# Kernel optimization log

Measured on AMD Instinct MI355X. Metric: run time of the kernel, lower is better.

The kernel has to match this reference:

```python
import jax, jax.numpy as jnp
import numpy as np

N, F, H, C, E = 100000, 128, 64, 16, 1000000


def _prop(x, src, dst, w):
    # gather source features, scale by edge weight, scatter-add to destinations
    msgs = x[src] * w[:, None]  # [E, H]
    return jax.ops.segment_sum(msgs, dst, num_segments=N)


def _gru(x, h, W_ih, W_hh, b_ih, b_hh):
    gi = x @ W_ih.T + b_ih  # [N, 3H]
    gh = h @ W_hh.T + b_hh
    i_r, i_z, i_n = jnp.split(gi, 3, axis=1)
    h_r, h_z, h_n = jnp.split(gh, 3, axis=1)
    r = jax.nn.sigmoid(i_r + h_r)
    z = jax.nn.sigmoid(i_z + h_z)
    n = jnp.tanh(i_n + r * h_n)
    return (1.0 - z) * n + z * h


def setup_inputs() -> dict:
    key = jax.random.key(0)
    ks = jax.random.split(key, 20)
    s = 0.05
    inp = {
        'x': jax.random.normal(ks[0], (N, F), jnp.float32),
        'edge_index': jax.random.randint(ks[1], (2, E), 0, N),
        'edge_weight': jax.random.uniform(ks[2], (E,), jnp.float32),
        'edge_index_re': jax.random.randint(ks[3], (2, E), 0, N),
        'edge_weight_re': jax.random.uniform(ks[4], (E,), jnp.float32),
        'W_first': jax.random.normal(ks[5], (H, F), jnp.float32) * s,
        'b_first': jnp.zeros((H,), jnp.float32),
        'W_con1': jax.random.normal(ks[6], (H, 2 * H), jnp.float32) * s,
        'b_con1': jnp.zeros((H,), jnp.float32),
        'W_con2': jax.random.normal(ks[7], (H, 2 * H), jnp.float32) * s,
        'b_con2': jnp.zeros((H,), jnp.float32),
        'W_lin1': jax.random.normal(ks[8], (H, H), jnp.float32) * s,
        'b_lin1': jnp.zeros((H,), jnp.float32),
        'W_out': jax.random.normal(ks[9], (C, H), jnp.float32) * s,
        'b_out': jnp.zeros((C,), jnp.float32),
        'W_ih': jax.random.normal(ks[10], (3 * H, H), jnp.float32) * s,
        'W_hh': jax.random.normal(ks[11], (3 * H, H), jnp.float32) * s,
        'b_ih': jnp.zeros((3 * H,), jnp.float32),
        'b_hh': jnp.zeros((3 * H,), jnp.float32),
    }
    return inp


def reference(x, edge_index, edge_weight, edge_index_re, edge_weight_re,
              W_first, b_first, W_con1, b_con1, W_con2, b_con2,
              W_lin1, b_lin1, W_out, b_out, W_ih, W_hh, b_ih, b_hh):
    src, dst = edge_index[0], edge_index[1]
    src_r, dst_r = edge_index_re[0], edge_index_re[1]

    x = x @ W_first.T + b_first  # [N, H]; dropout is identity at inference
    h = x

    x1 = _prop(x, src, dst, edge_weight)
    x2 = _prop(x, src_r, dst_r, edge_weight_re)
    x = jnp.concatenate([x1, x2], axis=1) @ W_con1.T + b_con1
    x = _gru(x, h, W_ih, W_hh, b_ih, b_hh)
    x = x @ W_lin1.T + b_lin1

    x1 = _prop(x, src, dst, edge_weight)
    x2 = _prop(x, src_r, dst_r, edge_weight_re)
    x = jnp.concatenate([x1, x2], axis=1) @ W_con2.T + b_con2
    x = _gru(x, h, W_ih, W_hh, b_ih, b_hh)
    x = x @ W_out.T + b_out
    return jax.nn.log_softmax(x, axis=-1)
```

## Files before the change

kernel.cpp:

```cpp
#include <hip/hip_runtime.h>

#define NN 100000
#define FF 128
#define HH 64
#define CC 16
#define EE 1000000
#define NSEG (2*NN)
#define BSH 11
#define BKD  (1 << BSH)
#define NBUK ((NSEG + BKD - 1) / BKD)
#define EPB 4096
#define P1BLK ((2*EE + EPB - 1) / EPB)
#define PRE_TOT (192*128 + 192 + 192*64 + 64*128 + 64*64 + 16*64)
#define PRE_BLK ((PRE_TOT + 255)/256)
#define LIN_TILES ((NN + 31)/32)
#define LINB ((LIN_TILES + 3)/4)

typedef __bf16 bf16;
typedef __attribute__((ext_vector_type(8))) __bf16 bf16x8;
typedef __attribute__((ext_vector_type(4))) __bf16 bf16x4;
typedef __attribute__((ext_vector_type(4))) float f32x4;
typedef __attribute__((ext_vector_type(2))) float f32x2;

__device__ __forceinline__ float fsig(float t)  { return 1.0f/(1.0f+__expf(-t)); }
__device__ __forceinline__ float ftanh(float t) { return 1.0f - 2.0f/(__expf(2.0f*t)+1.0f); }

__device__ __forceinline__ unsigned pack_sw(int s, float w) {
    unsigned short u = __builtin_bit_cast(unsigned short, (bf16)w);
    return ((unsigned)s << 15) | (u & 0x7FFFu);
}

__device__ __forceinline__ void precomp_body(int idx,
                               const float* __restrict__ W_ih, const float* __restrict__ b_ih,
                               const float* __restrict__ Wc1,  const float* __restrict__ bc1,
                               const float* __restrict__ Wc2,  const float* __restrict__ bc2,
                               const float* __restrict__ W_hh, const float* __restrict__ W_first,
                               const float* __restrict__ W_lin1, const float* __restrict__ W_out,
                               bf16* __restrict__ W1bf, float* __restrict__ b1,
                               bf16* __restrict__ W2bf, float* __restrict__ b2,
                               bf16* __restrict__ Whbf, bf16* __restrict__ Wfbf,
                               bf16* __restrict__ Wlbf, bf16* __restrict__ Wobf)
{
    const int t0 = 192*128;
    const int t1 = t0 + 192;
    const int t2 = t1 + 192*64;
    const int t3 = t2 + 64*128;
    const int t4 = t3 + 64*64;
    const int t5 = t4 + 16*64;
    if (idx < t0) {
        int j = idx >> 7, k = idx & 127;
        float s1 = 0.f, s2 = 0.f;
        for (int m=0; m<64; ++m) {
            float wih = W_ih[j*64+m];
            s1 += wih * Wc1[m*128+k];
            s2 += wih * Wc2[m*128+k];
        }
        W1bf[idx] = (bf16)s1; W2bf[idx] = (bf16)s2;
    } else if (idx < t1) {
        int j = idx - t0;
        float s1 = b_ih[j], s2 = b_ih[j];
        for (int m=0; m<64; ++m) {
            float wih = W_ih[j*64+m];
            s1 += wih * bc1[m];
            s2 += wih * bc2[m];
        }
        b1[j] = s1; b2[j] = s2;
    } else if (idx < t2) {
        int i = idx - t1;  Whbf[i] = (bf16)W_hh[i];
    } else if (idx < t3) {
        int i = idx - t2;  Wfbf[i] = (bf16)W_first[i];
    } else if (idx < t4) {
        int i = idx - t3;  Wlbf[i] = (bf16)W_lin1[i];
    } else if (idx < t5) {
        int i = idx - t4;  Wobf[i] = (bf16)W_out[i];
    }
}

__global__ __launch_bounds__(256) void count_precomp_kernel(
    const int* __restrict__ ei, const int* __restrict__ ei_re, int* __restrict__ bkcnt,
    const float* __restrict__ W_ih, const float* __restrict__ b_ih,
    const float* __restrict__ Wc1,  const float* __restrict__ bc1,
    const float* __restrict__ Wc2,  const float* __restrict__ bc2,
    const float* __restrict__ W_hh, const float* __restrict__ W_first,
    const float* __restrict__ W_lin1, const float* __restrict__ W_out,
    bf16* __restrict__ W1bf, float* __restrict__ b1,
    bf16* __restrict__ W2bf, float* __restrict__ b2,
    bf16* __restrict__ Whbf, bf16* __restrict__ Wfbf,
    bf16* __restrict__ Wlbf, bf16* __restrict__ Wobf)
{
    __shared__ int hist[NBUK];
    const int t = threadIdx.x;
    if (blockIdx.x < P1BLK) {
        for (int i=t; i<NBUK; i+=256) hist[i] = 0;
        __syncthreads();
        const long e0 = (long)blockIdx.x * EPB;
        #pragma unroll
        for (int it=0; it<16; ++it) {
            long e = e0 + it*256 + t;
            int d = -1;
            if (e < EE)        d = ei[EE + e];
            else if (e < 2*EE) d = NN + ei_re[EE + (e - EE)];
            if (d >= 0) atomicAdd(&hist[d >> BSH], 1);
        }
        __syncthreads();
        for (int i=t; i<NBUK; i+=256) if (hist[i]) atomicAdd(&bkcnt[i], hist[i]);
    } else {
        int idx = (blockIdx.x - P1BLK)*256 + t;
        precomp_body(idx, W_ih, b_ih, Wc1, bc1, Wc2, bc2, W_hh, W_first, W_lin1, W_out,
                     W1bf, b1, W2bf, b2, Whbf, Wfbf, Wlbf, Wobf);
    }
}

__global__ void bucket_scan_kernel(const int* __restrict__ bkcnt,
                                   int* __restrict__ bkbase, int* __restrict__ bkcur,
                                   int* __restrict__ rp)
{
    __shared__ int sc[128];
    const int t = threadIdx.x;
    int v = (t < NBUK) ? bkcnt[t] : 0;
    sc[t] = v;
    __syncthreads();
    #pragma unroll
    for (int off=1; off<128; off<<=1) {
        int x = (t>=off) ? sc[t-off] : 0;
        __syncthreads();
        sc[t] += x;
        __syncthreads();
    }
    int excl = sc[t] - v;
    if (t < NBUK) { bkbase[t] = excl; bkcur[t] = excl; }
    if (t == NBUK-1) bkbase[NBUK] = sc[t];
    if (t == 0) rp[NSEG] = 2*EE;
}

__global__ __launch_bounds__(256) void fillA_kernel(const int* __restrict__ ei,
                                                    const float* __restrict__ ew,
                                                    const int* __restrict__ ei_re,
                                                    const float* __restrict__ ew_re,
                                                    int* __restrict__ bkcur,
                                                    int* __restrict__ tmp_d,
                                                    unsigned* __restrict__ tmp_p)
{
    __shared__ int hist[NBUK];
    __shared__ int base[NBUK];
    const int t = threadIdx.x;
    for (int i=t; i<NBUK; i+=256) hist[i] = 0;
    __syncthreads();
    const long e0 = (long)blockIdx.x * EPB;
    int pr[16];
    #pragma unroll
    for (int it=0; it<16; ++it) {
        long e = e0 + it*256 + t;
        int d = -1;
        if (e < EE)        d = ei[EE + e];
        else if (e < 2*EE) d = NN + ei_re[EE + (e - EE)];
        if (d >= 0) {
            int b = d >> BSH;
            int r = atomicAdd(&hist[b], 1);
            pr[it] = (b << 16) | r;
        } else pr[it] = -1;
    }
    __syncthreads();
    for (int i=t; i<NBUK; i+=256) base[i] = atomicAdd(&bkcur[i], hist[i]);
    __syncthreads();
    #pragma unroll
    for (int it=0; it<16; ++it) {
        if (pr[it] < 0) continue;
        long e = e0 + it*256 + t;
        int d, s; float w;
        if (e < EE) { d = ei[EE+e]; s = ei[e]; w = ew[e]; }
        else { long j = e - EE; d = NN + ei_re[EE+j]; s = ei_re[j]; w = ew_re[j]; }
        int pos = base[pr[it] >> 16] + (pr[it] & 0xFFFF);
        tmp_d[pos] = d;
        tmp_p[pos] = pack_sw(s, w);
    }
}

__global__ __launch_bounds__(1024) void fillB_lin_kernel(
    const int* __restrict__ bkbase,
    const int* __restrict__ tmp_d, const unsigned* __restrict__ tmp_p,
    unsigned* __restrict__ edata, int* __restrict__ rp,
    const float* __restrict__ X, const bf16* __restrict__ Wf,
    const float* __restrict__ bfirst, float* __restrict__ Y, bf16* __restrict__ Ybf)
{
    __shared__ __align__(16) char smem[4*32*136*2];
    const int t = threadIdx.x;
    if (blockIdx.x < NBUK) {
        int* cntL  = (int*)smem;
        int* scanL = (int*)(smem + BKD*4);
        const int b  = blockIdx.x;
        const int d0 = b << BSH;
        const int dn = min(BKD, NSEG - d0);
        const int p0 = bkbase[b];
        const int p1 = bkbase[b+1];
        for (int i=t; i<BKD; i+=1024) cntL[i] = 0;
        __syncthreads();
        for (int pos = p0 + t; pos < p1; pos += 1024)
            atomicAdd(&cntL[tmp_d[pos] - d0], 1);
        __syncthreads();
        int a0 = cntL[2*t], a1 = cntL[2*t+1];
        int ps = a0 + a1;
        scanL[t] = ps;
        __syncthreads();
        #pragma unroll
        for (int off=1; off<1024; off<<=1) {
            int x = (t>=off) ? scanL[t-off] : 0;
            __syncthreads();
            scanL[t] += x;
            __syncthreads();
        }
        int g0 = p0 + scanL[t] - ps;
        int g1 = g0 + a0;
        if (2*t   < dn) rp[d0 + 2*t]   = g0;
        if (2*t+1 < dn) rp[d0 + 2*t+1] = g1;
        cntL[2*t]   = g0;
        cntL[2*t+1] = g1;
        __syncthreads();
        for (int pos = p0 + t; pos < p1; pos += 1024) {
            int d = tmp_d[pos];
            int p = atomicAdd(&cntL[d - d0], 1);
            edata[p] = tmp_p[pos];
        }
    } else {
        const int lb   = blockIdx.x - NBUK;
        const int sub  = t >> 8;
        const int tt   = t & 255;
        const int tile = lb*4 + sub;
        const bool valid = tile < LIN_TILES;
        const int tb = tile * 32;
        const int w = tt >> 6, lane = tt & 63, col = lane & 15, quad = lane >> 4;
        bf16* Alds = (bf16*)smem + sub*(32*136);
        bf16x8 B[4];
        #pragma unroll
        for (int ks=0; ks<4; ++ks)
            B[ks] = *(const bf16x8*)&Wf[(16*w+col)*128 + ks*32 + quad*8];
        const float bv = bfirst[16*w + col];
        const int m_st = tt >> 3, c_in = tt & 7;
        if (valid) {
            const float4* rx = (const float4*)&X[(long)(tb+m_st)*FF];
            #pragma unroll
            for (int it=0; it<4; ++it) {
                int cc = c_in + it*8;
                float4 v = rx[cc];
                bf16x4 bvv = {(bf16)v.x,(bf16)v.y,(bf16)v.z,(bf16)v.w};
                *(bf16x4*)&Alds[m_st*136 + cc*4] = bvv;
            }
        }
        __syncthreads();
        f32x4 acc[2] = {{0.f,0.f,0.f,0.f},{0.f,0.f,0.f,0.f}};
        #pragma unroll
        for (int ks=0; ks<4; ++ks)
            #pragma unroll
            for (int mt=0; mt<2; ++mt) {
                bf16x8 a = *(const bf16x8*)&Alds[(mt*16+col)*136 + ks*32+quad*8];
                acc[mt] = __builtin_amdgcn_mfma_f32_16x16x32_bf16(a, B[ks], acc[mt], 0,0,0);
            }
        if (valid) {
            #pragma unroll
            for (int mt=0; mt<2; ++mt)
                #pragma unroll
                for (int r=0; r<4; ++r) {
                    long n = tb + mt*16 + quad*4 + r;
                    float val = acc[mt][r] + bv;
                    Y  [n*HH + 16*w+col] = val;
                    Ybf[n*HH + 16*w+col] = (bf16)val;
                }
        }
    }
}

__global__ __launch_bounds__(256) void csr_prop_kernel(const bf16* __restrict__ X,
    const int* __restrict__ rp, const unsigned* __restrict__ edata,
    bf16* __restrict__ x1, bf16* __restrict__ x2)
{
    int s = blockIdx.x*4 + (threadIdx.x>>6);
    if (s >= NSEG) return;
    const int lane = threadIdx.x & 63;
    const int q  = lane >> 4;
    const int fl = lane & 15;
    const unsigned foff = 8u*(unsigned)fl;
    const int e0 = rp[s], e1 = rp[s+1];
    const char* Xb = (const char*)X;
    const char* Eb = (const char*)edata;

    f32x2 acc01 = {0.f, 0.f}, acc23 = {0.f, 0.f};
    int eq = e0 + q;
    unsigned eqb = 4u*(unsigned)eq;
    for (int base = e0; base < e1; base += 16, eq += 16, eqb += 64u) {
        const int rem = e1 - eq;
        #pragma unroll
        for (int j=0; j<4; ++j) {
            unsigned p = *(const unsigned*)(Eb + (eqb + 16u*(unsigned)j));
            const bool v = (4*j < rem);
            float w = v ? __uint_as_float((p & 0x7FFFu) << 16) : 0.f;
            unsigned voff = v ? (((p >> 8) & 0xFFFFFF80u) | foff) : foff;
            uint2 d = *(const uint2*)(Xb + voff);
            f32x2 lo = { __uint_as_float(d.x << 16), __uint_as_float(d.x & 0xFFFF0000u) };
            f32x2 hi = { __uint_as_float(d.y << 16), __uint_as_float(d.y & 0xFFFF0000u) };
            f32x2 w2 = { w, w };
            acc01 += w2 * lo;
            acc23 += w2 * hi;
        }
    }
    float a0 = acc01.x, a1 = acc01.y, a2 = acc23.x, a3 = acc23.y;
    a0 += __shfl_xor(a0, 32); a0 += __shfl_xor(a0, 16);
    a1 += __shfl_xor(a1, 32); a1 += __shfl_xor(a1, 16);
    a2 += __shfl_xor(a2, 32); a2 += __shfl_xor(a2, 16);
    a3 += __shfl_xor(a3, 32); a3 += __shfl_xor(a3, 16);
    if (q == 0) {
        bf16* o = (s < NN) ? &x1[(long)s*HH] : &x2[(long)(s-NN)*HH];
        bf16x4 ov = {(bf16)a0, (bf16)a1, (bf16)a2, (bf16)a3};
        *(bf16x4*)&o[4*fl] = ov;
    }
}

template<int MODE>
__global__ __launch_bounds__(256, 2) void layer_fused_kernel(
    const bf16* __restrict__ X1, const bf16* __restrict__ X2,
    const float* __restrict__ H, const bf16* __restrict__ Hbf,
    const bf16* __restrict__ Wg, const float* __restrict__ bg,
    const bf16* __restrict__ Wh, const float* __restrict__ bh,
    const bf16* __restrict__ Ws, const float* __restrict__ bs,
    bf16* __restrict__ Obf, float* __restrict__ Of)
{
    const int t    = threadIdx.x;
    const int w    = t >> 6;
    const int lane = t & 63;
    const int col  = lane & 15;
    const int quad = lane >> 4;

    bf16x8 Bg[3][4];
    bf16x8 Bh[3][2];
    float bgv[3], bhv[3];
    #pragma unroll
    for (int jt=0; jt<3; ++jt) {
        int J = jt*64 + 16*w + col;
        #pragma unroll
        for (int ks=0; ks<4; ++ks)
            Bg[jt][ks] = *(const bf16x8*)&Wg[J*128 + ks*32 + quad*8];
        #pragma unroll
        for (int ks=0; ks<2; ++ks)
            Bh[jt][ks] = *(const bf16x8*)&Wh[J*64 + ks*32 + quad*8];
        bgv[jt] = bg[J];
        bhv[jt] = bh[J];
    }

    bf16x8 B2[2];
    float b2s;
    if constexpr (MODE == 0) {
        #pragma unroll
        for (int ks=0; ks<2; ++ks)
            B2[ks] = *(const bf16x8*)&Ws[(16*w+col)*64 + ks*32 + quad*8];
        b2s = bs[16*w + col];
    } else {
        #pragma unroll
        for (int ks=0; ks<2; ++ks)
            B2[ks] = *(const bf16x8*)&Ws[col*64 + ks*32 + quad*8];
        b2s = bs[col];
    }

    __shared__ bf16 Alds[32][200];
    __shared__ bf16 Glds[32][72];

    const int m_st = t >> 3;
    const int c_in = t & 7;

    for (int tb = blockIdx.x*32; tb < NN; tb += gridDim.x*32) {
        {
            long n = tb + m_st;
            *(bf16x8*)&Alds[m_st][c_in*8]       = *(const bf16x8*)&X1[n*HH + c_in*8];
            *(bf16x8*)&Alds[m_st][64 + c_in*8]  = *(const bf16x8*)&X2[n*HH + c_in*8];
            *(bf16x8*)&Alds[m_st][128 + c_in*8] = *(const bf16x8*)&Hbf[n*HH + c_in*8];
        }
        __syncthreads();

        f32x4 accg[2][3];
        f32x4 acch[2][3];
        #pragma unroll
        for (int mt=0; mt<2; ++mt)
            #pragma unroll
            for (int jt=0; jt<3; ++jt) {
                accg[mt][jt] = (f32x4){0.f,0.f,0.f,0.f};
                acch[mt][jt] = (f32x4){0.f,0.f,0.f,0.f};
            }

        #pragma unroll
        for (int ks=0; ks<4; ++ks) {
            #pragma unroll
            for (int mt=0; mt<2; ++mt) {
                bf16x8 a = *(const bf16x8*)&Alds[mt*16 + col][ks*32 + quad*8];
                #pragma unroll
                for (int jt=0; jt<3; ++jt)
                    accg[mt][jt] = __builtin_amdgcn_mfma_f32_16x16x32_bf16(
                        a, Bg[jt][ks], accg[mt][jt], 0, 0, 0);
            }
        }
        #pragma unroll
        for (int ks=0; ks<2; ++ks) {
            #pragma unroll
            for (int mt=0; mt<2; ++mt) {
                bf16x8 a = *(const bf16x8*)&Alds[mt*16 + col][128 + ks*32 + quad*8];
                #pragma unroll
                for (int jt=0; jt<3; ++jt)
                    acch[mt][jt] = __builtin_amdgcn_mfma_f32_16x16x32_bf16(
                        a, Bh[jt][ks], acch[mt][jt], 0, 0, 0);
            }
        }

        const int c = 16*w + col;
        #pragma unroll
        for (int mt=0; mt<2; ++mt) {
            #pragma unroll
            for (int r=0; r<4; ++r) {
                long n = tb + mt*16 + quad*4 + r;
                float gr = accg[mt][0][r] + bgv[0];
                float gz = accg[mt][1][r] + bgv[1];
                float gn = accg[mt][2][r] + bgv[2];
                float hr = acch[mt][0][r] + bhv[0];
                float hz = acch[mt][1][r] + bhv[1];
                float hn = acch[mt][2][r] + bhv[2];
                float rr = fsig(gr + hr);
                float zz = fsig(gz + hz);
                float nv = ftanh(gn + rr*hn);
                float hv = H[n*HH + c];
                Glds[mt*16 + quad*4 + r][c] = (bf16)((1.0f - zz)*nv + zz*hv);
            }
        }
        __syncthreads();

        if constexpr (MODE == 0) {
            f32x4 acc2[2] = {{0.f,0.f,0.f,0.f},{0.f,0.f,0.f,0.f}};
            #pragma unroll
            for (int ks=0; ks<2; ++ks)
                #pragma unroll
                for (int mt=0; mt<2; ++mt) {
                    bf16x8 a = *(const bf16x8*)&Glds[mt*16+col][ks*32+quad*8];
                    acc2[mt] = __builtin_amdgcn_mfma_f32_16x16x32_bf16(a, B2[ks], acc2[mt], 0,0,0);
                }
            #pragma unroll
            for (int mt=0; mt<2; ++mt)
                #pragma unroll
                for (int r=0; r<4; ++r)
                    Obf[(long)(tb+mt*16+quad*4+r)*HH + 16*w+col] = (bf16)(acc2[mt][r] + b2s);
        } else {
            if (w < 2) {
                f32x4 acc2 = {0.f,0.f,0.f,0.f};
                #pragma unroll
                for (int ks=0; ks<2; ++ks) {
                    bf16x8 a = *(const bf16x8*)&Glds[w*16+col][ks*32+quad*8];
                    acc2 = __builtin_amdgcn_mfma_f32_16x16x32_bf16(a, B2[ks], acc2, 0,0,0);
                }
                #pragma unroll
                for (int r=0; r<4; ++r) {
                    long n = tb + w*16 + quad*4 + r;
                    float val = acc2[r] + b2s;
                    float m = val;
                    #pragma unroll
                    for (int off=8; off>0; off>>=1) m = fmaxf(m, __shfl_xor(m, off, 16));
                    float ex = __expf(val - m);
                    float ssum = ex;
                    #pragma unroll
                    for (int off=8; off>0; off>>=1) ssum += __shfl_xor(ssum, off, 16);
                    Of[n*CC + col] = val - m - __logf(ssum);
                }
            }
        }
    }
}

extern "C" void kernel_launch(void* const* d_in, const int* in_sizes, int n_in,
                              void* d_out, int out_size, void* d_ws, size_t ws_size,
                              hipStream_t stream)
{
    const float* x       = (const float*)d_in[0];
    const int*   ei      = (const int*)  d_in[1];
    const float* ew      = (const float*)d_in[2];
    const int*   ei_re   = (const int*)  d_in[3];
    const float* ew_re   = (const float*)d_in[4];
    const float* W_first = (const float*)d_in[5];
    const float* b_first = (const float*)d_in[6];
    const float* W_con1  = (const float*)d_in[7];
    const float* b_con1  = (const float*)d_in[8];
    const float* W_con2  = (const float*)d_in[9];
    const float* b_con2  = (const float*)d_in[10];
    const float* W_lin1  = (const float*)d_in[11];
    const float* b_lin1  = (const float*)d_in[12];
    const float* W_out   = (const float*)d_in[13];
    const float* b_out   = (const float*)d_in[14];
    const float* W_ih    = (const float*)d_in[15];
    const float* W_hh    = (const float*)d_in[16];
    const float* b_ih    = (const float*)d_in[17];
    const float* b_hh    = (const float*)d_in[18];
    float* out = (float*)d_out;

    float* h    = (float*)d_ws;
    bf16*  x1b  = (bf16*)(h + (long)NN*HH);
    bf16*  x2b  = x1b + (long)NN*HH;
    bf16*  hbf  = x2b + (long)NN*HH;
    bf16*  hAbf = hbf + (long)NN*HH;
    float* b1 = (float*)(hAbf + (long)NN*HH);
    float* b2 = b1 + 192;
    bf16*  W1bf = (bf16*)(b2 + 192);
    bf16*  W2bf = W1bf + 192*128;
    bf16*  Whbf = W2bf + 192*128;
    bf16*  Wfbf = Whbf + 192*64;
    bf16*  Wlbf = Wfbf + 64*128;
    bf16*  Wobf = Wlbf + 64*64;
    unsigned* edata = (unsigned*)(Wobf + 16*64);
    int*   rp     = (int*)(edata + 2*EE);
    int*   bkcnt  = rp + NSEG + 1;
    int*   bkbase = bkcnt + NBUK;
    int*   bkcur  = bkbase + NBUK + 1;
    int*      tmp_d = (int*)x1b;
    unsigned* tmp_p = (unsigned*)x2b;

    hipMemsetAsync(bkcnt, 0, (size_t)NBUK*sizeof(int), stream);
    count_precomp_kernel<<<P1BLK + PRE_BLK, 256, 0, stream>>>(
        ei, ei_re, bkcnt,
        W_ih, b_ih, W_con1, b_con1, W_con2, b_con2, W_hh, W_first, W_lin1, W_out,
        W1bf, b1, W2bf, b2, Whbf, Wfbf, Wlbf, Wobf);

    bucket_scan_kernel<<<1, 128, 0, stream>>>(bkcnt, bkbase, bkcur, rp);

    fillA_kernel<<<P1BLK, 256, 0, stream>>>(ei, ew, ei_re, ew_re, bkcur, tmp_d, tmp_p);

    fillB_lin_kernel<<<NBUK + LINB, 1024, 0, stream>>>(
        bkbase, tmp_d, tmp_p, edata, rp, x, Wfbf, b_first, h, hbf);

    csr_prop_kernel<<<(NSEG + 3)/4, 256, 0, stream>>>(hbf, rp, edata, x1b, x2b);

    layer_fused_kernel<0><<<1024, 256, 0, stream>>>(x1b, x2b, h, hbf, W1bf, b1, Whbf, b_hh,
                                                    Wlbf, b_lin1, hAbf, nullptr);

    csr_prop_kernel<<<(NSEG + 3)/4, 256, 0, stream>>>(hAbf, rp, edata, x1b, x2b);

    layer_fused_kernel<1><<<1024, 256, 0, stream>>>(x1b, x2b, h, hbf, W2bf, b2, Whbf, b_hh,
                                                    Wobf, b_out, nullptr, out);
}
```

Baseline: 380.5 us.

## Fold bucket scan into fill kernels, grid-stride CSR prop, stage H in LDS

Removes the single-block bucket_scan launch by having each fillA and fillB block redo the 98-entry prefix scan over bucket counts locally. This saves a kernel launch and a serial dependency at the cost of redundant per-block scans and extra barriers. The CSR propagation kernel becomes a grid-stride loop with a fixed 2048-block grid instead of one wave per segment row. The GRU layer now loads fp32 H once into LDS and converts it to bf16 there, replacing separate reads of the bf16 and fp32 copies of h.

```diff
diff --git a/kernel.cpp b/kernel.cpp
--- a/kernel.cpp
+++ b/kernel.cpp
@@ -15,6 +15,7 @@
 #define PRE_BLK ((PRE_TOT + 255)/256)
 #define LIN_TILES ((NN + 31)/32)
 #define LINB ((LIN_TILES + 3)/4)
+#define CSRB 2048
 
 typedef __bf16 bf16;
 typedef __attribute__((ext_vector_type(8))) __bf16 bf16x8;
@@ -111,40 +112,22 @@
     }
 }
 
-__global__ void bucket_scan_kernel(const int* __restrict__ bkcnt,
-                                   int* __restrict__ bkbase, int* __restrict__ bkcur,
-                                   int* __restrict__ rp)
-{
-    __shared__ int sc[128];
-    const int t = threadIdx.x;
-    int v = (t < NBUK) ? bkcnt[t] : 0;
-    sc[t] = v;
-    __syncthreads();
-    #pragma unroll
-    for (int off=1; off<128; off<<=1) {
-        int x = (t>=off) ? sc[t-off] : 0;
-        __syncthreads();
-        sc[t] += x;
-        __syncthreads();
-    }
-    int excl = sc[t] - v;
-    if (t < NBUK) { bkbase[t] = excl; bkcur[t] = excl; }
-    if (t == NBUK-1) bkbase[NBUK] = sc[t];
-    if (t == 0) rp[NSEG] = 2*EE;
-}
-
 __global__ __launch_bounds__(256) void fillA_kernel(const int* __restrict__ ei,
                                                     const float* __restrict__ ew,
                                                     const int* __restrict__ ei_re,
                                                     const float* __restrict__ ew_re,
+                                                    const int* __restrict__ bkcnt,
                                                     int* __restrict__ bkcur,
                                                     int* __restrict__ tmp_d,
                                                     unsigned* __restrict__ tmp_p)
 {
     __shared__ int hist[NBUK];
     __shared__ int base[NBUK];
+    __shared__ int sc[128];
     const int t = threadIdx.x;
     for (int i=t; i<NBUK; i+=256) hist[i] = 0;
+    int v = 0;
+    if (t < 128) { v = (t < NBUK) ? bkcnt[t] : 0; sc[t] = v; }
     __syncthreads();
     const long e0 = (long)blockIdx.x * EPB;
     int pr[16];
@@ -161,7 +144,17 @@
         } else pr[it] = -1;
     }
     __syncthreads();
-    for (int i=t; i<NBUK; i+=256) base[i] = atomicAdd(&bkcur[i], hist[i]);
+    #pragma unroll
+    for (int off=1; off<128; off<<=1) {
+        int x = 0;
+        if (t >= off && t < 128) x = sc[t-off];
+        __syncthreads();
+        if (t < 128) sc[t] += x;
+        __syncthreads();
+    }
+    if (t < 128 && t < NBUK) base[t] = sc[t] - v;
+    __syncthreads();
+    for (int i=t; i<NBUK; i+=256) base[i] += atomicAdd(&bkcur[i], hist[i]);
     __syncthreads();
     #pragma unroll
     for (int it=0; it<16; ++it) {
@@ -177,7 +170,7 @@
 }
 
 __global__ __launch_bounds__(1024) void fillB_lin_kernel(
-    const int* __restrict__ bkbase,
+    const int* __restrict__ bkcnt,
     const int* __restrict__ tmp_d, const unsigned* __restrict__ tmp_p,
     unsigned* __restrict__ edata, int* __restrict__ rp,
     const float* __restrict__ X, const bf16* __restrict__ Wf,
@@ -188,13 +181,24 @@
     if (blockIdx.x < NBUK) {
         int* cntL  = (int*)smem;
         int* scanL = (int*)(smem + BKD*4);
+        int* sc98  = (int*)(smem + BKD*4 + 4096);
         const int b  = blockIdx.x;
         const int d0 = b << BSH;
         const int dn = min(BKD, NSEG - d0);
-        const int p0 = bkbase[b];
-        const int p1 = bkbase[b+1];
+        if (b == 0 && t == 0) rp[NSEG] = 2*EE;
+        if (t < 128) sc98[t] = (t < NBUK) ? bkcnt[t] : 0;
         for (int i=t; i<BKD; i+=1024) cntL[i] = 0;
         __syncthreads();
+        #pragma unroll
+        for (int off=1; off<128; off<<=1) {
+            int x = 0;
+            if (t >= off && t < 128) x = sc98[t-off];
+            __syncthreads();
+            if (t < 128) sc98[t] += x;
+            __syncthreads();
+        }
+        const int p0 = (b == 0) ? 0 : sc98[b-1];
+        const int p1 = sc98[b];
         for (int pos = p0 + t; pos < p1; pos += 1024)
             atomicAdd(&cntL[tmp_d[pos] - d0], 1);
         __syncthreads();
@@ -273,51 +277,51 @@
     const int* __restrict__ rp, const unsigned* __restrict__ edata,
     bf16* __restrict__ x1, bf16* __restrict__ x2)
 {
-    int s = blockIdx.x*4 + (threadIdx.x>>6);
-    if (s >= NSEG) return;
     const int lane = threadIdx.x & 63;
     const int q  = lane >> 4;
     const int fl = lane & 15;
     const unsigned foff = 8u*(unsigned)fl;
-    const int e0 = rp[s], e1 = rp[s+1];
     const char* Xb = (const char*)X;
     const char* Eb = (const char*)edata;
 
-    f32x2 acc01 = {0.f, 0.f}, acc23 = {0.f, 0.f};
-    int eq = e0 + q;
-    unsigned eqb = 4u*(unsigned)eq;
-    for (int base = e0; base < e1; base += 16, eq += 16, eqb += 64u) {
-        const int rem = e1 - eq;
-        #pragma unroll
-        for (int j=0; j<4; ++j) {
-            unsigned p = *(const unsigned*)(Eb + (eqb + 16u*(unsigned)j));
-            const bool v = (4*j < rem);
-            float w = v ? __uint_as_float((p & 0x7FFFu) << 16) : 0.f;
-            unsigned voff = v ? (((p >> 8) & 0xFFFFFF80u) | foff) : foff;
-            uint2 d = *(const uint2*)(Xb + voff);
-            f32x2 lo = { __uint_as_float(d.x << 16), __uint_as_float(d.x & 0xFFFF0000u) };
-            f32x2 hi = { __uint_as_float(d.y << 16), __uint_as_float(d.y & 0xFFFF0000u) };
-            f32x2 w2 = { w, w };
-            acc01 += w2 * lo;
-            acc23 += w2 * hi;
-        }
-    }
-    float a0 = acc01.x, a1 = acc01.y, a2 = acc23.x, a3 = acc23.y;
-    a0 += __shfl_xor(a0, 32); a0 += __shfl_xor(a0, 16);
-    a1 += __shfl_xor(a1, 32); a1 += __shfl_xor(a1, 16);
-    a2 += __shfl_xor(a2, 32); a2 += __shfl_xor(a2, 16);
-    a3 += __shfl_xor(a3, 32); a3 += __shfl_xor(a3, 16);
-    if (q == 0) {
-        bf16* o = (s < NN) ? &x1[(long)s*HH] : &x2[(long)(s-NN)*HH];
-        bf16x4 ov = {(bf16)a0, (bf16)a1, (bf16)a2, (bf16)a3};
-        *(bf16x4*)&o[4*fl] = ov;
+    for (int s = blockIdx.x*4 + (threadIdx.x>>6); s < NSEG; s += gridDim.x*4) {
+        const int e0 = rp[s], e1 = rp[s+1];
+        f32x2 acc01 = {0.f, 0.f}, acc23 = {0.f, 0.f};
+        int eq = e0 + q;
+        unsigned eqb = 4u*(unsigned)eq;
+        for (int base = e0; base < e1; base += 16, eq += 16, eqb += 64u) {
+            const int rem = e1 - eq;
+            #pragma unroll
+            for (int j=0; j<4; ++j) {
+                unsigned p = *(const unsigned*)(Eb + (eqb + 16u*(unsigned)j));
+                const bool v = (4*j < rem);
+                float w = v ? __uint_as_float((p & 0x7FFFu) << 16) : 0.f;
+                unsigned voff = v ? (((p >> 8) & 0xFFFFFF80u) | foff) : foff;
+                uint2 d = *(const uint2*)(Xb + voff);
+                f32x2 lo = { __uint_as_float(d.x << 16), __uint_as_float(d.x & 0xFFFF0000u) };
+                f32x2 hi = { __uint_as_float(d.y << 16), __uint_as_float(d.y & 0xFFFF0000u) };
+                f32x2 w2 = { w, w };
+                acc01 += w2 * lo;
+                acc23 += w2 * hi;
+            }
+        }
+        float a0 = acc01.x, a1 = acc01.y, a2 = acc23.x, a3 = acc23.y;
+        a0 += __shfl_xor(a0, 32); a0 += __shfl_xor(a0, 16);
+        a1 += __shfl_xor(a1, 32); a1 += __shfl_xor(a1, 16);
+        a2 += __shfl_xor(a2, 32); a2 += __shfl_xor(a2, 16);
+        a3 += __shfl_xor(a3, 32); a3 += __shfl_xor(a3, 16);
+        if (q == 0) {
+            bf16* o = (s < NN) ? &x1[(long)s*HH] : &x2[(long)(s-NN)*HH];
+            bf16x4 ov = {(bf16)a0, (bf16)a1, (bf16)a2, (bf16)a3};
+            *(bf16x4*)&o[4*fl] = ov;
+        }
     }
 }
 
 template<int MODE>
 __global__ __launch_bounds__(256, 2) void layer_fused_kernel(
     const bf16* __restrict__ X1, const bf16* __restrict__ X2,
-    const float* __restrict__ H, const bf16* __restrict__ Hbf,
+    const float* __restrict__ H,
     const bf16* __restrict__ Wg, const float* __restrict__ bg,
     const bf16* __restrict__ Wh, const float* __restrict__ bh,
     const bf16* __restrict__ Ws, const float* __restrict__ bs,
@@ -359,8 +363,9 @@
         b2s = bs[col];
     }
 
-    __shared__ bf16 Alds[32][200];
-    __shared__ bf16 Glds[32][72];
+    __shared__ bf16  Alds[32][200];
+    __shared__ bf16  Glds[32][72];
+    __shared__ float Hlds[32][66];
 
     const int m_st = t >> 3;
     const int c_in = t & 7;
@@ -368,9 +373,15 @@
     for (int tb = blockIdx.x*32; tb < NN; tb += gridDim.x*32) {
         {
             long n = tb + m_st;
-            *(bf16x8*)&Alds[m_st][c_in*8]       = *(const bf16x8*)&X1[n*HH + c_in*8];
-            *(bf16x8*)&Alds[m_st][64 + c_in*8]  = *(const bf16x8*)&X2[n*HH + c_in*8];
-            *(bf16x8*)&Alds[m_st][128 + c_in*8] = *(const bf16x8*)&Hbf[n*HH + c_in*8];
+            *(bf16x8*)&Alds[m_st][c_in*8]      = *(const bf16x8*)&X1[n*HH + c_in*8];
+            *(bf16x8*)&Alds[m_st][64 + c_in*8] = *(const bf16x8*)&X2[n*HH + c_in*8];
+            const float4* rh = (const float4*)&H[n*HH];
+            float4 a = rh[c_in*2], b4 = rh[c_in*2+1];
+            bf16x8 hb = {(bf16)a.x,(bf16)a.y,(bf16)a.z,(bf16)a.w,
+                         (bf16)b4.x,(bf16)b4.y,(bf16)b4.z,(bf16)b4.w};
+            *(bf16x8*)&Alds[m_st][128 + c_in*8] = hb;
+            *(float4*)&Hlds[m_st][c_in*8]     = a;
+            *(float4*)&Hlds[m_st][c_in*8 + 4] = b4;
         }
         __syncthreads();
 
@@ -412,7 +423,6 @@
         for (int mt=0; mt<2; ++mt) {
             #pragma unroll
             for (int r=0; r<4; ++r) {
-                long n = tb + mt*16 + quad*4 + r;
                 float gr = accg[mt][0][r] + bgv[0];
                 float gz = accg[mt][1][r] + bgv[1];
                 float gn = accg[mt][2][r] + bgv[2];
@@ -422,7 +432,7 @@
                 float rr = fsig(gr + hr);
                 float zz = fsig(gz + hz);
                 float nv = ftanh(gn + rr*hn);
-                float hv = H[n*HH + c];
+                float hv = Hlds[mt*16 + quad*4 + r][c];
                 Glds[mt*16 + quad*4 + r][c] = (bf16)((1.0f - zz)*nv + zz*hv);
             }
         }
@@ -509,31 +519,28 @@
     unsigned* edata = (unsigned*)(Wobf + 16*64);
     int*   rp     = (int*)(edata + 2*EE);
     int*   bkcnt  = rp + NSEG + 1;
-    int*   bkbase = bkcnt + NBUK;
-    int*   bkcur  = bkbase + NBUK + 1;
+    int*   bkcur  = bkcnt + NBUK;
     int*      tmp_d = (int*)x1b;
     unsigned* tmp_p = (unsigned*)x2b;
 
-    hipMemsetAsync(bkcnt, 0, (size_t)NBUK*sizeof(int), stream);
+    hipMemsetAsync(bkcnt, 0, (size_t)(2*NBUK)*sizeof(int), stream);
     count_precomp_kernel<<<P1BLK + PRE_BLK, 256, 0, stream>>>(
         ei, ei_re, bkcnt,
         W_ih, b_ih, W_con1, b_con1, W_con2, b_con2, W_hh, W_first, W_lin1, W_out,
         W1bf, b1, W2bf, b2, Whbf, Wfbf, Wlbf, Wobf);
 
-    bucket_scan_kernel<<<1, 128, 0, stream>>>(bkcnt, bkbase, bkcur, rp);
-
-    fillA_kernel<<<P1BLK, 256, 0, stream>>>(ei, ew, ei_re, ew_re, bkcur, tmp_d, tmp_p);
+    fillA_kernel<<<P1BLK, 256, 0, stream>>>(ei, ew, ei_re, ew_re, bkcnt, bkcur, tmp_d, tmp_p);
 
     fillB_lin_kernel<<<NBUK + LINB, 1024, 0, stream>>>(
-        bkbase, tmp_d, tmp_p, edata, rp, x, Wfbf, b_first, h, hbf);
-
-    csr_prop_kernel<<<(NSEG + 3)/4, 256, 0, stream>>>(hbf, rp, edata, x1b, x2b);
-
-    layer_fused_kernel<0><<<1024, 256, 0, stream>>>(x1b, x2b, h, hbf, W1bf, b1, Whbf, b_hh,
+        bkcnt, tmp_d, tmp_p, edata, rp, x, Wfbf, b_first, h, hbf);
+
+    csr_prop_kernel<<<CSRB, 256, 0, stream>>>(hbf, rp, edata, x1b, x2b);
+
+    layer_fused_kernel<0><<<1024, 256, 0, stream>>>(x1b, x2b, h, W1bf, b1, Whbf, b_hh,
                                                     Wlbf, b_lin1, hAbf, nullptr);
 
-    csr_prop_kernel<<<(NSEG + 3)/4, 256, 0, stream>>>(hAbf, rp, edata, x1b, x2b);
-
-    layer_fused_kernel<1><<<1024, 256, 0, stream>>>(x1b, x2b, h, hbf, W2bf, b2, Whbf, b_hh,
+    csr_prop_kernel<<<CSRB, 256, 0, stream>>>(hAbf, rp, edata, x1b, x2b);
+
+    layer_fused_kernel<1><<<1024, 256, 0, stream>>>(x1b, x2b, h, W2bf, b2, Whbf, b_hh,
                                                     Wobf, b_out, nullptr, out);
 }
```

Result: faster. 370.1 us (-2.7%).
